# Performance work log

Hardware: AMD Instinct MI355X
Metric: run time of the kernel (lower is better)

Reference implementation:

```python
import math
import jax, jax.numpy as jnp
import numpy as np

EPS = 1e-5  # BatchNorm1d default eps


def setup_inputs() -> dict:
    key = jax.random.key(0)
    ks = jax.random.split(key, 8)
    B, H, N, L, CD = 16, 64, 64, 16384, 3
    dt_min, dt_max = 1e-3, 1e-1
    # DSSM parameters (as in __init__)
    log_dt = jax.random.uniform(ks[0], (H,)) * (math.log(dt_max) - math.log(dt_min)) + math.log(dt_min)
    C_ri = jax.random.normal(ks[1], (H, N, 2))  # view_as_real of complex C
    log_A_real = jnp.log(0.5 * jnp.ones((H, N)))
    A_imag = math.pi * jnp.tile(jnp.arange(N, dtype=jnp.float32)[None, :], (H, 1))
    D = jax.random.normal(ks[2], (H,))
    # FiLM adaptor: Linear(cond_dim, 2*H)
    film_w = jax.random.normal(ks[3], (2 * H, CD)) / np.sqrt(CD)
    film_b = jnp.zeros((2 * H,))
    u = jax.random.normal(ks[4], (B, H, L))
    cond = jax.random.uniform(ks[5], (B, CD))
    length = jax.random.randint(ks[6], (B,), 1, L + 1)
    return dict(u=u, cond=cond, length=length, log_dt=log_dt, C_ri=C_ri,
                log_A_real=log_A_real, A_imag=A_imag, D=D,
                film_w=film_w, film_b=film_b)


def _dssm(u, length, log_dt, C_ri, log_A_real, A_imag, D):
    # u: (B, H, L). Length-agnostic equivalent of the torch length-bucketed path:
    # mask input beyond each example's length (bucket slicing u[idxs,:,:l]),
    # do one full-length linear FFT conv, then zero output beyond the length
    # (out[idxs,:,:l] = y leaves the tail at zero).
    B, H, L = u.shape
    dt = jnp.exp(log_dt)                       # (H,)
    C = C_ri[..., 0] + 1j * C_ri[..., 1]       # (H, N) complex
    A = -jnp.exp(log_A_real) + 1j * A_imag     # (H, N) complex
    dtA = A * dt[:, None]                      # (H, N)
    t = jnp.arange(L, dtype=jnp.float32)
    P = jnp.exp(dtA[:, :, None] * t)           # (H, N, L) complex
    Ck = C * (jnp.exp(dtA) - 1.0) / A          # (H, N)
    K = 2.0 * jnp.einsum('hn,hnl->hl', Ck, P).real  # (H, L) real kernel
    mask = (t[None, :] < length[:, None]).astype(u.dtype)  # (B, L)
    um = u * mask[:, None, :]
    n = 2 * L  # rfft size; linear conv of length-L signals has length 2L-1 <= 2L
    y = jnp.fft.irfft(jnp.fft.rfft(um, n=n) * jnp.fft.rfft(K, n=n)[None], n=n)[..., :L]
    y = (y + um * D[:, None]) * mask[:, None, :]
    return y


def _film(y, cond, film_w, film_b):
    # BatchNorm1d(affine=False), training-mode batch stats over (B, L) per channel
    H = y.shape[1]
    gb = cond @ film_w.T + film_b               # (B, 2H)
    g, b = gb[:, :H, None], gb[:, H:, None]
    mean = y.mean(axis=(0, 2))
    var = y.var(axis=(0, 2))                    # biased variance (torch BN normalization)
    yn = (y - mean[None, :, None]) * jax.lax.rsqrt(var[None, :, None] + EPS)
    return yn * g + b


def reference(u, cond, length, log_dt, C_ri, log_A_real, A_imag, D, film_w, film_b):
    y = _dssm(u, length, log_dt, C_ri, log_A_real, A_imag, D)
    y = _film(y, cond, film_w, film_b)
    y = jnp.tanh(y)
    return u + y  # residual connection around the conditioned SSM block
```

## Files before the change

### kernel.cpp

```cpp
#include <hip/hip_runtime.h>
#include <hip/hip_bf16.h>

typedef __hip_bfloat16 bf16;
typedef __attribute__((ext_vector_type(8))) short s16x8;
typedef __attribute__((ext_vector_type(4))) float f32x4;

#define SWZY(c) ((((c) ^ ((c) >> 3) ^ ((c) >> 4)) & 7) << 4)
#define GB(c)  ((((c) ^ ((c) >> 3) ^ ((c) >> 5)) & 7))
#define DWP(ml, c) (((ml) & 3) | (((((ml) >> 2) ^ GB(c)) & 7) << 2))

__device__ __forceinline__ unsigned short f2b(float x){
    __hip_bfloat16 h = __float2bfloat16(x);
    return __builtin_bit_cast(unsigned short, h);
}
__device__ __forceinline__ float b2f(unsigned short s){
    unsigned int u = (unsigned int)s << 16;
    return __builtin_bit_cast(float, u);
}

__global__ __launch_bounds__(256) void k0_setup(const float* __restrict__ log_dt,
        const float* __restrict__ C_ri, const float* __restrict__ log_A_real,
        const float* __restrict__ A_imag, const float* __restrict__ Dp,
        float* __restrict__ rLtab, float* __restrict__ rStab,
        short* __restrict__ Qh,
        short* __restrict__ Pmh, short* __restrict__ Pml,
        short* __restrict__ Klh, short* __restrict__ Kll)
{
    __shared__ float arr[64][65];
    __shared__ float a0[64];
    __shared__ float kd[64];
    int h = blockIdx.x;
    int tid = threadIdx.x;
    int n = tid & 63, g = tid >> 6;
    int hn = h * 64 + n;
    double dtd  = exp((double)log_dt[h]);
    float  Aref = -expf(log_A_real[hn]);
    double Ared = (double)Aref;
    double Aimd = (double)A_imag[hn];
    double adt  = Aimd * dtd;
    float  mdt  = (float)(Ared * dtd);
    auto cexp = [&](float e, float& re, float& im){
        double a = adt * (double)e;
        double k = floor(a * 0.15915494309189535);
        float ang = (float)(a - k * 6.283185307179586);
        float si, co;
        __sincosf(ang, &si, &co);
        float mag = expf(mdt * e);
        re = mag * co; im = mag * si;
    };
    float rre, rim; cexp(1.f, rre, rim);
    float Cre = C_ri[2 * hn], Cim = C_ri[2 * hn + 1];
    float emre = rre - 1.f, emim = rim;
    float inva2 = 1.f / (Aref * Aref + (float)(Aimd * Aimd));
    float qre_ = (emre * Aref + emim * (float)Aimd) * inva2;
    float qim_ = (emim * Aref - emre * (float)Aimd) * inva2;
    float ckre = Cre * qre_ - Cim * qim_;
    float ckim = Cre * qim_ + Cim * qre_;
    {
        short* q0 = Qh + (size_t)h * 8192 + (2 * n) * 64;
        short* q1 = q0 + 64;
        for (int t = 16 * g; t < 16 * g + 16; ++t) {
            float pre, pim; cexp((float)(63 - t), pre, pim);
            q0[t] = (short)f2b(pre);
            q1[t] = (short)f2b(pim);
        }
    }
    if (g == 0) {
        float pre, pim; cexp(64.f, pre, pim);
        rLtab[2 * hn] = pre; rLtab[2 * hn + 1] = pim;
    }
    if (g == 1) {
        float pre, pim; cexp(2048.f, pre, pim);
        rStab[2 * hn] = pre; rStab[2 * hn + 1] = pim;
    }
    if (g == 2) a0[n] = 2.f * ckre;
    {
        short* pmh = Pmh + (size_t)h * 8192;
        short* pml = Pml + (size_t)h * 8192;
        for (int j = 16 * g; j < 16 * g + 16; ++j) {
            float pre, pim; cexp((float)(j + 1), pre, pim);
            float wre = 2.f * (ckre * pre - ckim * pim);
            float wim = 2.f * (ckre * pim + ckim * pre);
            unsigned short h0 = f2b(wre), h1 = f2b(-wim);
            pmh[j * 128 + 2 * n]     = (short)h0;
            pml[j * 128 + 2 * n]     = (short)f2b(wre - b2f(h0));
            pmh[j * 128 + 2 * n + 1] = (short)h1;
            pml[j * 128 + 2 * n + 1] = (short)f2b(-wim - b2f(h1));
            arr[j][n] = wre;
        }
    }
    __syncthreads();
    if (tid < 64) {
        int d = tid;
        float s = 0.f;
        if (d == 0) { for (int k = 0; k < 64; ++k) s += a0[k]; }
        else        { for (int k = 0; k < 64; ++k) s += arr[d - 1][k]; }
        kd[d] = s;
    }
    __syncthreads();
    {
        float Dh = Dp[h];
        short* klh = Klh + (size_t)h * 4096 + n * 64;
        short* kll = Kll + (size_t)h * 4096 + n * 64;
        for (int t = 16 * g; t < 16 * g + 16; ++t) {
            if (t <= n) {
                float v = kd[n - t] + ((t == n) ? Dh : 0.f);
                unsigned short h0 = f2b(v);
                klh[t] = (short)h0;
                kll[t] = (short)f2b(v - b2f(h0));
            } else { klh[t] = 0; kll[t] = 0; }
        }
    }
}

__global__ __launch_bounds__(256, 2) void k_fused(const float* __restrict__ u,
        const int* __restrict__ length,
        const float* __restrict__ rLtab, const float* __restrict__ rStab,
        const short* __restrict__ Qh,
        const short* __restrict__ Pmh, const short* __restrict__ Pml,
        const short* __restrict__ Klh, const short* __restrict__ Kll,
        bf16* __restrict__ y, double* __restrict__ stats)
{
    __shared__ __align__(16) unsigned char lds[32768];
    int bh = blockIdx.x;
    int b = bh >> 6, h = bh & 63;
    int tid = threadIdx.x;
    int w = tid >> 6, lane = tid & 63;
    int lo = lane & 15, hi = lane >> 4;
    int len = length[b];
    const float* ub = u + (size_t)bh * 16384;

    s16x8 xh[4][2], xl[4][2];
    #pragma unroll
    for (int ct = 0; ct < 4; ++ct) {
        int c = w * 64 + ct * 16 + lo;
        #pragma unroll
        for (int kt = 0; kt < 2; ++kt) {
            int gidx = c * 64 + kt * 32 + hi * 8;
            float4 v0 = *(const float4*)(ub + gidx);
            float4 v1 = *(const float4*)(ub + gidx + 4);
            float xv[8] = {v0.x, v0.y, v0.z, v0.w, v1.x, v1.y, v1.z, v1.w};
            s16x8 fh, fl;
            #pragma unroll
            for (int e = 0; e < 8; ++e) {
                float xm = (gidx + e < len) ? xv[e] : 0.f;
                unsigned short h0 = f2b(xm);
                fh[e] = (short)h0;
                fl[e] = (short)f2b(xm - b2f(h0));
            }
            xh[ct][kt] = fh;
            xl[ct][kt] = fl;
        }
    }

    f32x4 acc[4][4];
    #pragma unroll
    for (int ct = 0; ct < 4; ++ct)
        #pragma unroll
        for (int jt = 0; jt < 4; ++jt)
            acc[ct][jt] = f32x4{0.f, 0.f, 0.f, 0.f};
    {
        const short* klhb = Klh + (size_t)h * 4096;
        const short* kllb = Kll + (size_t)h * 4096;
        #pragma unroll
        for (int kt = 0; kt < 2; ++kt) {
            #pragma unroll
            for (int jt = 0; jt < 4; ++jt) {
                s16x8 kfh = *(const s16x8*)(klhb + (jt * 16 + lo) * 64 + kt * 32 + hi * 8);
                s16x8 kfl = *(const s16x8*)(kllb + (jt * 16 + lo) * 64 + kt * 32 + hi * 8);
                #pragma unroll
                for (int ct = 0; ct < 4; ++ct) {
                    acc[ct][jt] = __builtin_amdgcn_mfma_f32_16x16x32_bf16(xh[ct][kt], kfh, acc[ct][jt], 0, 0, 0);
                    acc[ct][jt] = __builtin_amdgcn_mfma_f32_16x16x32_bf16(xh[ct][kt], kfl, acc[ct][jt], 0, 0, 0);
                    acc[ct][jt] = __builtin_amdgcn_mfma_f32_16x16x32_bf16(xl[ct][kt], kfh, acc[ct][jt], 0, 0, 0);
                }
            }
        }
    }

    auto gemm1 = [&](int hh){
        const short* qb = Qh + (size_t)h * 8192 + (hh * 64) * 64;
        #pragma unroll
        for (int mt = 0; mt < 4; ++mt) {
            s16x8 q0 = *(const s16x8*)(qb + (mt * 16 + lo) * 64 + hi * 8);
            s16x8 q1 = *(const s16x8*)(qb + (mt * 16 + lo) * 64 + 32 + hi * 8);
            #pragma unroll
            for (int ct = 0; ct < 4; ++ct) {
                f32x4 sc = f32x4{0.f, 0.f, 0.f, 0.f};
                sc = __builtin_amdgcn_mfma_f32_16x16x32_bf16(q0, xh[ct][0], sc, 0, 0, 0);
                sc = __builtin_amdgcn_mfma_f32_16x16x32_bf16(q1, xh[ct][1], sc, 0, 0, 0);
                int c = w * 64 + ct * 16 + lo;
                int ml0 = 8 * mt + 2 * hi;
                unsigned int p0 = (unsigned)f2b(sc[0]) | ((unsigned)f2b(sc[1]) << 16);
                unsigned int p1 = (unsigned)f2b(sc[2]) | ((unsigned)f2b(sc[3]) << 16);
                unsigned long long pp = (unsigned long long)p0 | ((unsigned long long)p1 << 32);
                *(unsigned long long*)(lds + c * 128 + DWP(ml0, c) * 4) = pp;
            }
        }
    };
    auto gemm3 = [&](int hh){
        const short* pmhb = Pmh + (size_t)h * 8192 + hh * 64;
        const short* pmlb = Pml + (size_t)h * 8192 + hh * 64;
        #pragma unroll
        for (int kt2 = 0; kt2 < 2; ++kt2) {
            s16x8 af[4];
            #pragma unroll
            for (int ct = 0; ct < 4; ++ct) {
                int c = w * 64 + ct * 16 + lo;
                int blk = (4 * kt2 + hi) ^ GB(c);
                af[ct] = *(const s16x8*)(lds + c * 128 + blk * 16);
            }
            #pragma unroll
            for (int jt = 0; jt < 4; ++jt) {
                s16x8 pfh = *(const s16x8*)(pmhb + (jt * 16 + lo) * 128 + kt2 * 32 + hi * 8);
                s16x8 pfl = *(const s16x8*)(pmlb + (jt * 16 + lo) * 128 + kt2 * 32 + hi * 8);
                #pragma unroll
                for (int ct = 0; ct < 4; ++ct) {
                    acc[ct][jt] = __builtin_amdgcn_mfma_f32_16x16x32_bf16(af[ct], pfh, acc[ct][jt], 0, 0, 0);
                    acc[ct][jt] = __builtin_amdgcn_mfma_f32_16x16x32_bf16(af[ct], pfl, acc[ct][jt], 0, 0, 0);
                }
            }
        }
    };
    auto scan = [&](int hh){
        int m = tid >> 3, s = tid & 7;
        int gm = (h * 64 + hh * 32 + m) * 2;
        float r64re = rLtab[gm], r64im = rLtab[gm + 1];
        float pre = rStab[gm],  pim = rStab[gm + 1];
        float ere = 0.f, eim = 0.f;
        #pragma unroll
        for (int i = 0; i < 32; ++i) {
            int c = 32 * s + i;
            unsigned int v = *(const unsigned int*)(lds + c * 128 + DWP(m, c) * 4);
            float vre = b2f((unsigned short)v);
            float vim = b2f((unsigned short)(v >> 16));
            float nre = fmaf(r64re, ere, fmaf(-r64im, eim, vre));
            eim = fmaf(r64re, eim, fmaf(r64im, ere, vim));
            ere = nre;
        }
        #pragma unroll
        for (int d = 1; d < 8; d <<= 1) {
            float orr = __shfl(ere, (lane - d) & 63, 64);
            float oii = __shfl(eim, (lane - d) & 63, 64);
            if (s >= d) {
                float nre = fmaf(pre, orr, fmaf(-pim, oii, ere));
                eim = fmaf(pre, oii, fmaf(pim, orr, eim));
                ere = nre;
            }
            float t2 = pre * pre - pim * pim;
            pim = 2.f * pre * pim;
            pre = t2;
        }
        float cire = __shfl(ere, (lane - 1) & 63, 64);
        float ciim = __shfl(eim, (lane - 1) & 63, 64);
        if (s == 0) { cire = 0.f; ciim = 0.f; }
        #pragma unroll
        for (int i = 0; i < 32; ++i) {
            int c = 32 * s + i;
            unsigned char* p = lds + c * 128 + DWP(m, c) * 4;
            unsigned int v = *(const unsigned int*)p;
            float vre = b2f((unsigned short)v);
            float vim = b2f((unsigned short)(v >> 16));
            *(unsigned int*)p = (unsigned)f2b(cire) | ((unsigned)f2b(ciim) << 16);
            float nre = fmaf(r64re, cire, fmaf(-r64im, ciim, vre));
            ciim = fmaf(r64re, ciim, fmaf(r64im, cire, vim));
            cire = nre;
        }
    };

    gemm1(0);
    __syncthreads();
    scan(0);
    __syncthreads();
    gemm3(0);
    gemm1(1);
    __syncthreads();
    scan(1);
    __syncthreads();
    gemm3(1);

    #pragma unroll
    for (int ct = 0; ct < 4; ++ct) {
        #pragma unroll
        for (int jt = 0; jt < 4; ++jt) {
            int j = jt * 16 + lo;
            #pragma unroll
            for (int rg = 0; rg < 4; ++rg) {
                int c = w * 64 + ct * 16 + hi * 4 + rg;
                *(unsigned short*)(lds + c * 128 + ((2 * j) ^ SWZY(c))) = f2b(acc[ct][jt][rg]);
            }
        }
    }
    __syncthreads();

    float s1 = 0.f, s2 = 0.f;
    short* yg = (short*)y + (size_t)bh * 16384;
    #pragma unroll
    for (int k = 0; k < 8; ++k) {
        int eidx = (k * 256 + tid) * 8;
        int row = eidx >> 6;
        int byt = ((eidx & 63) * 2) ^ SWZY(row);
        s16x8 yv = *(const s16x8*)(lds + row * 128 + byt);
        s16x8 o;
        #pragma unroll
        for (int e = 0; e < 8; ++e) {
            float vv = b2f((unsigned short)yv[e]);
            vv = (eidx + e < len) ? vv : 0.f;
            o[e] = (short)f2b(vv);
            s1 += vv;
            s2 = fmaf(vv, vv, s2);
        }
        *(s16x8*)(yg + eidx) = o;
    }
    #pragma unroll
    for (int off = 32; off > 0; off >>= 1) {
        s1 += __shfl_down(s1, off, 64);
        s2 += __shfl_down(s2, off, 64);
    }
    if (lane == 0) {
        atomicAdd(&stats[2 * h],     (double)s1);
        atomicAdd(&stats[2 * h + 1], (double)s2);
    }
}

__global__ __launch_bounds__(256) void k4_final(const float* __restrict__ u,
        const bf16* __restrict__ y, const float* __restrict__ cond,
        const float* __restrict__ fw, const float* __restrict__ fb,
        const double* __restrict__ stats, float* __restrict__ out)
{
    int tid = threadIdx.x;
    size_t idx8 = ((size_t)blockIdx.x * 256 + tid) * 8;
    int bh = (int)(idx8 >> 14);
    int b = bh >> 6, h = bh & 63;
    __shared__ float gg[2];
    if (tid == 0) {
        float g = fb[h], bb = fb[64 + h];
        #pragma unroll
        for (int k = 0; k < 3; ++k) {
            g  = fmaf(cond[b * 3 + k], fw[h * 3 + k], g);
            bb = fmaf(cond[b * 3 + k], fw[(64 + h) * 3 + k], bb);
        }
        gg[0] = g; gg[1] = bb;
    }
    __syncthreads();
    double inv = 1.0 / (16.0 * 16384.0);
    double mean_d = stats[2 * h] * inv;
    double var_d  = stats[2 * h + 1] * inv - mean_d * mean_d;
    float mean = (float)mean_d;
    float rstd = rsqrtf((float)var_d + 1e-5f);
    float gv = gg[0], bv = gg[1];
    float4 u0 = *(const float4*)(u + idx8);
    float4 u1 = *(const float4*)(u + idx8 + 4);
    s16x8 yv = *(const s16x8*)((const short*)y + idx8);
    float uv[8] = {u0.x, u0.y, u0.z, u0.w, u1.x, u1.y, u1.z, u1.w};
    float ov[8];
    #pragma unroll
    for (int e = 0; e < 8; ++e) {
        float z = fmaf((b2f((unsigned short)yv[e]) - mean) * rstd, gv, bv);
        ov[e] = uv[e] + tanhf(z);
    }
    *(float4*)(out + idx8)     = float4{ov[0], ov[1], ov[2], ov[3]};
    *(float4*)(out + idx8 + 4) = float4{ov[4], ov[5], ov[6], ov[7]};
}

extern "C" void kernel_launch(void* const* d_in, const int* in_sizes, int n_in,
                              void* d_out, int out_size, void* d_ws, size_t ws_size,
                              hipStream_t stream)
{
    const float* u           = (const float*)d_in[0];
    const float* cond        = (const float*)d_in[1];
    const int*   length      = (const int*)  d_in[2];
    const float* log_dt      = (const float*)d_in[3];
    const float* C_ri        = (const float*)d_in[4];
    const float* log_A_real  = (const float*)d_in[5];
    const float* A_imag      = (const float*)d_in[6];
    const float* D           = (const float*)d_in[7];
    const float* film_w      = (const float*)d_in[8];
    const float* film_b      = (const float*)d_in[9];
    float* out = (float*)d_out;

    char* w = (char*)d_ws;
    bf16*   y      = (bf16*)w;
    short*  Qh     = (short*)(w + 33554432);
    short*  Pmh    = (short*)(w + 34603008);
    short*  Pml    = (short*)(w + 35651584);
    short*  Klh    = (short*)(w + 36700160);
    short*  Kll    = (short*)(w + 37224448);
    float*  rLtab  = (float*)(w + 37748736);
    float*  rStab  = (float*)(w + 37781504);
    double* stats  = (double*)(w + 37814272);

    hipMemsetAsync(stats, 0, 1024, stream);
    hipLaunchKernelGGL(k0_setup, dim3(64),   dim3(256), 0, stream,
                       log_dt, C_ri, log_A_real, A_imag, D,
                       rLtab, rStab, Qh, Pmh, Pml, Klh, Kll);
    hipLaunchKernelGGL(k_fused,  dim3(1024), dim3(256), 0, stream,
                       u, length, rLtab, rStab, Qh, Pmh, Pml, Klh, Kll, y, stats);
    hipLaunchKernelGGL(k4_final, dim3(8192), dim3(256), 0, stream,
                       u, y, cond, film_w, film_b, stats, out);
}
```

Before: 107.9 us.

## Process both mode halves in one scan phase with doubled LDS buffer

Instead of two sequential gemm1/scan/gemm3 passes over 32 modes each, the kernel writes all 64 modes' chunk states into a doubled 64 KB LDS buffer and runs a single scan where each mode is handled by 4 threads over 64 chunks. This drops two barriers and halves the number of phases, while the cross-thread step multiplier becomes r^4096 to match the 64-chunk segments. The cost is a longer serial scan chain per thread and twice the LDS footprint, which may lower occupancy below the 2 blocks per CU requested in launch bounds.

```diff
diff --git a/kernel.cpp b/kernel.cpp
--- a/kernel.cpp
+++ b/kernel.cpp
@@ -70,7 +70,7 @@
         rLtab[2 * hn] = pre; rLtab[2 * hn + 1] = pim;
     }
     if (g == 1) {
-        float pre, pim; cexp(2048.f, pre, pim);
+        float pre, pim; cexp(4096.f, pre, pim);
         rStab[2 * hn] = pre; rStab[2 * hn + 1] = pim;
     }
     if (g == 2) a0[n] = 2.f * ckre;
@@ -121,7 +121,7 @@
         const short* __restrict__ Klh, const short* __restrict__ Kll,
         bf16* __restrict__ y, double* __restrict__ stats)
 {
-    __shared__ __align__(16) unsigned char lds[32768];
+    __shared__ __align__(16) unsigned char lds[65536];
     int bh = blockIdx.x;
     int b = bh >> 6, h = bh & 63;
     int tid = threadIdx.x;
@@ -177,9 +177,10 @@
             }
         }
     }
-
-    auto gemm1 = [&](int hh){
+    #pragma unroll
+    for (int hh = 0; hh < 2; ++hh) {
         const short* qb = Qh + (size_t)h * 8192 + (hh * 64) * 64;
+        unsigned char* base = lds + hh * 32768;
         #pragma unroll
         for (int mt = 0; mt < 4; ++mt) {
             s16x8 q0 = *(const s16x8*)(qb + (mt * 16 + lo) * 64 + hi * 8);
@@ -194,13 +195,66 @@
                 unsigned int p0 = (unsigned)f2b(sc[0]) | ((unsigned)f2b(sc[1]) << 16);
                 unsigned int p1 = (unsigned)f2b(sc[2]) | ((unsigned)f2b(sc[3]) << 16);
                 unsigned long long pp = (unsigned long long)p0 | ((unsigned long long)p1 << 32);
-                *(unsigned long long*)(lds + c * 128 + DWP(ml0, c) * 4) = pp;
-            }
-        }
-    };
-    auto gemm3 = [&](int hh){
+                *(unsigned long long*)(base + c * 128 + DWP(ml0, c) * 4) = pp;
+            }
+        }
+    }
+    __syncthreads();
+
+    {
+        int m = tid >> 2, s = tid & 3;
+        int hh = m >> 5, ml = m & 31;
+        unsigned char* base = lds + hh * 32768;
+        int gm = (h * 64 + m) * 2;
+        float r64re = rLtab[gm], r64im = rLtab[gm + 1];
+        float pre = rStab[gm],  pim = rStab[gm + 1];
+        float ere = 0.f, eim = 0.f;
+        #pragma unroll
+        for (int i = 0; i < 64; ++i) {
+            int c = 64 * s + i;
+            unsigned int v = *(const unsigned int*)(base + c * 128 + DWP(ml, c) * 4);
+            float vre = b2f((unsigned short)v);
+            float vim = b2f((unsigned short)(v >> 16));
+            float nre = fmaf(r64re, ere, fmaf(-r64im, eim, vre));
+            eim = fmaf(r64re, eim, fmaf(r64im, ere, vim));
+            ere = nre;
+        }
+        #pragma unroll
+        for (int d = 1; d < 4; d <<= 1) {
+            float orr = __shfl(ere, (lane - d) & 63, 64);
+            float oii = __shfl(eim, (lane - d) & 63, 64);
+            if (s >= d) {
+                float nre = fmaf(pre, orr, fmaf(-pim, oii, ere));
+                eim = fmaf(pre, oii, fmaf(pim, orr, eim));
+                ere = nre;
+            }
+            float t2 = pre * pre - pim * pim;
+            pim = 2.f * pre * pim;
+            pre = t2;
+        }
+        float cire = __shfl(ere, (lane - 1) & 63, 64);
+        float ciim = __shfl(eim, (lane - 1) & 63, 64);
+        if (s == 0) { cire = 0.f; ciim = 0.f; }
+        #pragma unroll
+        for (int i = 0; i < 64; ++i) {
+            int c = 64 * s + i;
+            unsigned char* p = base + c * 128 + DWP(ml, c) * 4;
+            unsigned int v = *(const unsigned int*)p;
+            float vre = b2f((unsigned short)v);
+            float vim = b2f((unsigned short)(v >> 16));
+            *(unsigned int*)p = (unsigned)f2b(cire) | ((unsigned)f2b(ciim) << 16);
+            float nre = fmaf(r64re, cire, fmaf(-r64im, ciim, vre));
+            ciim = fmaf(r64re, ciim, fmaf(r64im, cire, vim));
+            cire = nre;
+        }
+    }
+    __syncthreads();
+
+    #pragma unroll
+    for (int hh = 0; hh < 2; ++hh) {
         const short* pmhb = Pmh + (size_t)h * 8192 + hh * 64;
         const short* pmlb = Pml + (size_t)h * 8192 + hh * 64;
+        unsigned char* base = lds + hh * 32768;
         #pragma unroll
         for (int kt2 = 0; kt2 < 2; ++kt2) {
             s16x8 af[4];
@@ -208,7 +262,7 @@
             for (int ct = 0; ct < 4; ++ct) {
                 int c = w * 64 + ct * 16 + lo;
                 int blk = (4 * kt2 + hi) ^ GB(c);
-                af[ct] = *(const s16x8*)(lds + c * 128 + blk * 16);
+                af[ct] = *(const s16x8*)(base + c * 128 + blk * 16);
             }
             #pragma unroll
             for (int jt = 0; jt < 4; ++jt) {
@@ -221,64 +275,7 @@
                 }
             }
         }
-    };
-    auto scan = [&](int hh){
-        int m = tid >> 3, s = tid & 7;
-        int gm = (h * 64 + hh * 32 + m) * 2;
-        float r64re = rLtab[gm], r64im = rLtab[gm + 1];
-        float pre = rStab[gm],  pim = rStab[gm + 1];
-        float ere = 0.f, eim = 0.f;
-        #pragma unroll
-        for (int i = 0; i < 32; ++i) {
-            int c = 32 * s + i;
-            unsigned int v = *(const unsigned int*)(lds + c * 128 + DWP(m, c) * 4);
-            float vre = b2f((unsigned short)v);
-            float vim = b2f((unsigned short)(v >> 16));
-            float nre = fmaf(r64re, ere, fmaf(-r64im, eim, vre));
-            eim = fmaf(r64re, eim, fmaf(r64im, ere, vim));
-            ere = nre;
-        }
-        #pragma unroll
-        for (int d = 1; d < 8; d <<= 1) {
-            float orr = __shfl(ere, (lane - d) & 63, 64);
-            float oii = __shfl(eim, (lane - d) & 63, 64);
-            if (s >= d) {
-                float nre = fmaf(pre, orr, fmaf(-pim, oii, ere));
-                eim = fmaf(pre, oii, fmaf(pim, orr, eim));
-                ere = nre;
-            }
-            float t2 = pre * pre - pim * pim;
-            pim = 2.f * pre * pim;
-            pre = t2;
-        }
-        float cire = __shfl(ere, (lane - 1) & 63, 64);
-        float ciim = __shfl(eim, (lane - 1) & 63, 64);
-        if (s == 0) { cire = 0.f; ciim = 0.f; }
-        #pragma unroll
-        for (int i = 0; i < 32; ++i) {
-            int c = 32 * s + i;
-            unsigned char* p = lds + c * 128 + DWP(m, c) * 4;
-            unsigned int v = *(const unsigned int*)p;
-            float vre = b2f((unsigned short)v);
-            float vim = b2f((unsigned short)(v >> 16));
-            *(unsigned int*)p = (unsigned)f2b(cire) | ((unsigned)f2b(ciim) << 16);
-            float nre = fmaf(r64re, cire, fmaf(-r64im, ciim, vre));
-            ciim = fmaf(r64re, ciim, fmaf(r64im, cire, vim));
-            cire = nre;
-        }
-    };
-
-    gemm1(0);
-    __syncthreads();
-    scan(0);
-    __syncthreads();
-    gemm3(0);
-    gemm1(1);
-    __syncthreads();
-    scan(1);
-    __syncthreads();
-    gemm3(1);
-
+    }
     #pragma unroll
     for (int ct = 0; ct < 4; ++ct) {
         #pragma unroll
```

New measurement: 104.4 us. 1.03x faster.
